# Kernel optimization log

Measured on AMD Instinct MI355X. Metric: run time of the kernel, lower is better.

Reference implementation:

```python
import jax, jax.numpy as jnp
import numpy as np

B, L = 2, 2048
DIM, VOCAB, NL = 1024, 32000, 4
DSTATE, DCONV, EXPAND, HEADDIM = 128, 4, 2, 64
DIN = EXPAND * DIM            # 2048
H = DIN // HEADDIM            # 32 heads
CONVDIM = DIN + 2 * DSTATE    # 2304
DPROJ = 2 * DIN + 2 * DSTATE + H  # 4384
FFN = 4 * DIM                 # 4096
Q = 128                       # SSD chunk size
EPS = 1e-6


def _rms(x):
    return x * jax.lax.rsqrt(jnp.mean(x * x, axis=-1, keepdims=True) + EPS)


def _causal_conv(x, w, b):
    # x [B,L,C], depthwise causal conv, w [C,DCONV], b [C]
    y = jax.lax.conv_general_dilated(
        x.transpose(0, 2, 1), w[:, None, :], (1,), [(DCONV - 1, 0)],
        dimension_numbers=('NCH', 'OIH', 'NCH'), feature_group_count=CONVDIM)
    return (y + b[:, None]).transpose(0, 2, 1)


def _ssd(x, dt, A, Bm, Cm):
    # Exact selective scan h_t = h_{t-1}*exp(dt_t*A) + dt_t * x_t B_t ; y_t = C_t . h_t
    # computed in chunked (SSD) matmul form. x [b,l,h,p], dt [b,l,h], A [h], Bm/Cm [b,l,n]
    b, l, h, p = x.shape
    n = Bm.shape[-1]
    c = l // Q
    xr = x.reshape(b, c, Q, h, p)
    dtr = dt.reshape(b, c, Q, h)
    ar = (dt * A).reshape(b, c, Q, h)          # per-step log-decay (<= 0)
    Br = Bm.reshape(b, c, Q, n)
    Cr = Cm.reshape(b, c, Q, n)
    ca = jnp.cumsum(ar, axis=2)                # inclusive cumulative log-decay
    # ---- intra-chunk: causal decay-weighted 'attention' ----
    cah = ca.transpose(0, 1, 3, 2)             # [b,c,h,Q]
    idx = jnp.arange(Q)
    mask = idx[:, None] >= idx[None, :]
    diff = jnp.where(mask[None, None, None], cah[..., :, None] - cah[..., None, :], -jnp.inf)
    M = jnp.exp(diff)                          # [b,c,h,Q,Q]
    CB = jnp.einsum('bcin,bcjn->bcij', Cr, Br)
    T = CB[:, :, None] * M                     # [b,c,h,Q,Q]
    y_intra = jnp.einsum('bchij,bcjh,bcjhp->bcihp', T, dtr, xr)
    # ---- chunk-final states ----
    w = jnp.exp(ca[:, :, -1:, :] - ca) * dtr   # [b,c,Q,h]
    states = jnp.einsum('bcjh,bcjn,bcjhp->bchpn', w, Br, xr)
    chunk_decay = jnp.exp(ca[:, :, -1, :])     # [b,c,h]
    def step(s, inp):
        cd, st = inp
        prev = s
        s = s * cd[:, :, None, None] + st
        return s, prev
    s0 = jnp.zeros((b, h, p, n), x.dtype)
    _, s_prev = jax.lax.scan(step, s0, (chunk_decay.transpose(1, 0, 2),
                                        states.transpose(1, 0, 2, 3, 4)))
    s_prev = s_prev.transpose(1, 0, 2, 3, 4)   # [b,c,h,p,n] state entering each chunk
    y_inter = jnp.einsum('bcih,bcin,bchpn->bcihp', jnp.exp(ca), Cr, s_prev)
    return (y_intra + y_inter).reshape(b, l, h, p)


def _mamba(x, Wi, cw, cb, dtb, Alog, Dp, nw, Wo):
    bsz, sl, _ = x.shape
    zxbcdt = x @ Wi.T                          # [b,l,DPROJ]
    z = zxbcdt[..., :DIN]
    xBC = zxbcdt[..., DIN:DIN + CONVDIM]
    dtraw = zxbcdt[..., DIN + CONVDIM:]
    xBC = jax.nn.silu(_causal_conv(xBC, cw, cb))
    xs = xBC[..., :DIN]
    Bm = xBC[..., DIN:DIN + DSTATE]
    Cm = xBC[..., DIN + DSTATE:]
    dt = jax.nn.softplus(dtraw + dtb)
    A = -jnp.exp(Alog)
    x4 = xs.reshape(bsz, sl, H, HEADDIM)
    y = _ssd(x4, dt, A, Bm, Cm) + Dp[None, None, :, None] * x4
    y = y.reshape(bsz, sl, DIN)
    yg = y * jax.nn.silu(z)                    # gated RMSNorm (norm_before_gate=False)
    y = _rms(yg) * nw
    return y @ Wo.T


def _forward(tokens, embedding, lm_head_bias, in_proj_w, conv_w, conv_b,
             dt_bias, A_log, D, mnorm_w, out_proj_w, u_w, v_w, o_w):
    x = embedding[tokens]
    for li in range(NL):
        for _ in range(2):  # original applies each (mamba, ffn) pair twice
            x = _rms(x)
            x = x + _mamba(x, in_proj_w[li], conv_w[li], conv_b[li], dt_bias[li],
                           A_log[li], D[li], mnorm_w[li], out_proj_w[li])
            x = _rms(x)
            x = x + ((x @ u_w[li].T) * (x @ v_w[li].T)) @ o_w[li].T  # SGLU, dropout=0
    return x @ embedding.T + lm_head_bias      # tied lm_head


def setup_inputs():
    key = jax.random.key(0)
    ks = jax.random.split(key, 16)
    s = 0.02
    return {
        'tokens': jax.random.randint(ks[0], (B, L), 0, VOCAB),
        'embedding': jax.random.normal(ks[1], (VOCAB, DIM), jnp.float32) * s,
        'lm_head_bias': jnp.zeros((VOCAB,), jnp.float32),
        'in_proj_w': jax.random.normal(ks[2], (NL, DPROJ, DIM), jnp.float32) * s,
        'conv_w': jax.random.normal(ks[3], (NL, CONVDIM, DCONV), jnp.float32) * 0.2,
        'conv_b': jnp.zeros((NL, CONVDIM), jnp.float32),
        'dt_bias': jax.random.normal(ks[4], (NL, H), jnp.float32) * 0.3 - 3.0,
        'A_log': jnp.log(jax.random.uniform(ks[5], (NL, H), jnp.float32, 1.0, 16.0)),
        'D': jnp.ones((NL, H), jnp.float32) + 0.1 * jax.random.normal(ks[6], (NL, H), jnp.float32),
        'mnorm_w': jnp.ones((NL, DIN), jnp.float32),
        'out_proj_w': jax.random.normal(ks[7], (NL, DIM, DIN), jnp.float32) * s,
        'u_w': jax.random.normal(ks[8], (NL, FFN, DIM), jnp.float32) * s,
        'v_w': jax.random.normal(ks[9], (NL, FFN, DIM), jnp.float32) * s,
        'o_w': jax.random.normal(ks[10], (NL, DIM, FFN), jnp.float32) * s,
    }


def reference(tokens, embedding, lm_head_bias, in_proj_w, conv_w, conv_b,
              dt_bias, A_log, D, mnorm_w, out_proj_w, u_w, v_w, o_w):
    return _forward(tokens, embedding, lm_head_bias, in_proj_w, conv_w, conv_b,
                    dt_bias, A_log, D, mnorm_w, out_proj_w, u_w, v_w, o_w)
```

## Files before the change

### kernel.cpp

```cpp
#include <hip/hip_runtime.h>
#include <hip/hip_bf16.h>

#define BSZ 2
#define LSEQ 2048
#define DIM 1024
#define VOCAB 32000
#define NLAYER 4
#define DSTATE 128
#define DCONV 4
#define HEADDIM 64
#define DIN 2048
#define NH 32
#define CONVDIM 2304
#define DPROJ 4384
#define FFN 4096
#define QLEN 128
#define NTOK 4096
#define NCHUNK 32
#define CPB 16

#define SMEM_BYTES 147456
#define SMEM2 131072

using f32x4 = __attribute__((ext_vector_type(4))) float;
using f16   = _Float16;
using f16x4 = __attribute__((ext_vector_type(4))) _Float16;
using f16x8 = __attribute__((ext_vector_type(8))) _Float16;

__device__ __forceinline__ void gld16(const void* g, void* l) {
  __builtin_amdgcn_global_load_lds(
      (const __attribute__((address_space(1))) unsigned int*)g,
      (__attribute__((address_space(3))) unsigned int*)l, 16, 0, 0);
}

// ... 6 lines not shown
  const int nchx = nx / CW;
  const int per = CW * ny;
  const int ch = bid / per;
  if (ch < nchx) {
    int wi = bid - ch * per;
    bx = ch * CW + (wi & (CW - 1));
    by = wi / CW;
  } else {
    int tb = bid - nchx * per;
    int tw = nx - nchx * CW;
    bx = nchx * CW + (tb % tw);
    by = tb / tw;
  }
}

template <int MODE>
__global__ __launch_bounds__(512, 2) void gemm_p(
    const f16* __restrict__ A, const f16* __restrict__ Bu, const f16* __restrict__ Bv,
    float* __restrict__ Cf, f16* __restrict__ Gh, const float* __restrict__ bias,
    int N, int Ksub, int lda, int ldb, int ldc)
{
  extern __shared__ char smem[];
  const int tid  = threadIdx.x;
  const int lane = tid & 63;
  const int wid  = tid >> 6;
  int bx, by; swz_tiles(bx, by);
  const int m0 = by * 256;
  const int n0 = bx * 128;
  const size_t kbase = (size_t)blockIdx.z * Ksub;
  if (gridDim.z > 1) Cf += (size_t)blockIdx.z * (size_t)gridDim.y * 256 * ldc;

  const int NT  = Ksub >> 6;
  const int NTT = (MODE == 2) ? 2 * NT : NT;

  int arA[4], acA[4];
#pragma unroll
  for (int L = 0; L < 4; ++L) {
    int q = L * 512 + tid;
    int row = q >> 3;
    arA[L] = m0 + row;
    acA[L] = ((q & 7) ^ (row & 7)) << 3;
  }
  int brB[2], bcB[2];
#pragma unroll
  for (int L = 0; L < 2; ++L) {
    int q = L * 512 + tid;
    int row = q >> 3;
    int r = n0 + row; if (r > N - 1) r = N - 1;
    brB[L] = r;
    bcB[L] = ((q & 7) ^ (row & 7)) << 3;
  }

  auto stage = [&](int tt) {
    const int b = tt - (tt / 3) * 3;
    char* Ad = smem + b * 32768;
    char* Bd = smem + 98304 + b * 16384;
    int ta = tt;
    const f16* Bp = Bu;
    if (MODE == 2 && tt >= NT) { ta = tt - NT; Bp = Bv; }
    const int kb = ta << 6;
#pragma unroll
    for (int L = 0; L < 4; ++L)
      gld16(A + (size_t)arA[L] * lda + kbase + kb + acA[L], Ad + (L * 512 + tid) * 16);
#pragma unroll
    for (int L = 0; L < 2; ++L)
      gld16(Bp + (size_t)brB[L] * ldb + kbase + kb + bcB[L], Bd + (L * 512 + tid) * 16);
  };

  const int wm = (wid >> 1) << 6;
  const int wn = (wid & 1) << 6;
  const int fr = lane & 15;
  const int kg = lane >> 4;

  f32x4 accu[4][4] = {};
  f32x4 accv[4][4] = {};

  stage(0);
  stage(1);

  for (int t = 0; t < NTT; ++t) {
    const int b = t - (t / 3) * 3;
    if (t + 2 < NTT) {
      stage(t + 2);
      asm volatile("s_waitcnt vmcnt(12)" ::: "memory");
    } else if (t + 1 < NTT) {
      asm volatile("s_waitcnt vmcnt(6)" ::: "memory");
    } else {
      asm volatile("s_waitcnt vmcnt(0)" ::: "memory");
    }
    __builtin_amdgcn_s_barrier();
    asm volatile("" ::: "memory");
    const f16* Ab = (const f16*)(smem + b * 32768);
    const f16* Bb = (const f16*)(smem + 98304 + b * 16384);
#pragma unroll
    for (int s = 0; s < 2; ++s) {
      f16x8 af[4], bf[4];
#pragma unroll
      for (int j = 0; j < 4; ++j) {
        int row = wm + j * 16 + fr;
        int g = kg + s * 4;
        af[j] = *(const f16x8*)&Ab[row * 64 + ((g ^ (row & 7)) << 3)];
      }
#pragma unroll
      for (int i = 0; i < 4; ++i) {
        int row = wn + i * 16 + fr;
        int g = kg + s * 4;
        bf[i] = *(const f16x8*)&Bb[row * 64 + ((g ^ (row & 7)) << 3)];
      }
      __builtin_amdgcn_s_setprio(1);
      if (MODE == 2 && t >= NT) {
#pragma unroll
        for (int i = 0; i < 4; ++i)
#pragma unroll
          for (int j = 0; j < 4; ++j)
            accv[i][j] = __builtin_amdgcn_mfma_f32_16x16x32_f16(bf[i], af[j], accv[i][j], 0, 0, 0);
      } else {
#pragma unroll
        for (int i = 0; i < 4; ++i)
#pragma unroll
          for (int j = 0; j < 4; ++j)
            accu[i][j] = __builtin_amdgcn_mfma_f32_16x16x32_f16(bf[i], af[j], accu[i][j], 0, 0, 0);
      }
      __builtin_amdgcn_s_setprio(0);
    }
    asm volatile("" ::: "memory");
    __builtin_amdgcn_s_barrier();
    asm volatile("" ::: "memory");
  }

  const int c4 = kg << 2;
  if constexpr (MODE == 0) {
#pragma unroll
    for (int i = 0; i < 4; ++i) {
      const int col = n0 + wn + i * 16 + c4;
      if (col >= N) continue;
      f32x4 bv = bias ? *(const f32x4*)(bias + col) : f32x4{0, 0, 0, 0};
#pragma unroll
      for (int j = 0; j < 4; ++j) {
        const int row = m0 + wm + j * 16 + fr;
        *(f32x4*)(Cf + (size_t)row * ldc + col) = accu[i][j] + bv;
      }
    }
  } else {
#pragma unroll
    for (int i = 0; i < 4; ++i) {
      const int col = n0 + wn + i * 16 + c4;
#pragma unroll
      for (int j = 0; j < 4; ++j) {
        const int row = m0 + wm + j * 16 + fr;
        f16x4 h;
#pragma unroll
        for (int r = 0; r < 4; ++r)
          h[r] = (f16)(accu[i][j][r] * accv[i][j][r]);
        *(f16x4*)(Gh + (size_t)row * ldc + col) = h;
      }
    }
  }
}

__global__ __launch_bounds__(512, 2) void gemm_p2(
    const f16* __restrict__ A, const f16* __restrict__ B,
    float* __restrict__ Cf, const float* __restrict__ bias,
    int N, int Ksub, int lda, int ldb, int ldc)
{
  extern __shared__ char smem[];
  const int tid  = threadIdx.x;
  const int lane = tid & 63;
  const int wid  = tid >> 6;
  int bx, by; swz_tiles(bx, by);
  const int m0 = by * 256;
  const int n0 = bx * 256;
  const size_t kbase = (size_t)blockIdx.z * Ksub;
  if (gridDim.z > 1) Cf += (size_t)blockIdx.z * (size_t)gridDim.y * 256 * ldc;
  const int NT = Ksub >> 6;

  int arA[4], acA[4], brB[4], bcB[4];
#pragma unroll
  for (int L = 0; L < 4; ++L) {
    int q = L * 512 + tid;
    int row = q >> 3;
    arA[L] = m0 + row;
    acA[L] = ((q & 7) ^ (row & 7)) << 3;
    int r = n0 + row; if (r > N - 1) r = N - 1;
    brB[L] = r;
    bcB[L] = acA[L];
  }

  auto stage = [&](int tt) {
// ... 166 lines not shown
  for (int i = 0; i < 4; ++i) {
    const int col = n0 + wn + i * 16 + c4;
#pragma unroll
    for (int j = 0; j < 4; ++j) {
      const int row = m0 + wm + j * 16 + fr;
      f16x4 h;
#pragma unroll
      for (int r = 0; r < 4; ++r)
        h[r] = (f16)(accu[i][j][r] * accv[i][j][r]);
      *(f16x4*)(Gh + (size_t)row * FFN + col) = h;
    }
  }
}

template <bool DORMS>
__global__ __launch_bounds__(256) void reduce_rms(const float* __restrict__ parts,
                                                  const float* __restrict__ resid,
                                                  float* __restrict__ xn,
                                                  f16* __restrict__ outh, int np)
{
  const int row = blockIdx.x, tid = threadIdx.x;
  const size_t base = (size_t)row * DIM + tid * 4;
  f32x4 s = *(const f32x4*)(resid + base);
  for (int p = 0; p < np; ++p)
    s += *(const f32x4*)(parts + (size_t)p * (NTOK * DIM) + base);
  if constexpr (!DORMS) {
    f16x4 h;
#pragma unroll
    for (int c = 0; c < 4; ++c) h[c] = (f16)s[c];
    *(f16x4*)(outh + base) = h;
    return;
  }
  float ss = s[0] * s[0] + s[1] * s[1] + s[2] * s[2] + s[3] * s[3];
  for (int o = 32; o; o >>= 1) ss += __shfl_down(ss, o);
  __shared__ float red[4];
  if ((tid & 63) == 0) red[tid >> 6] = ss;
  __syncthreads();
  ss = red[0] + red[1] + red[2] + red[3];
  const float sc = rsqrtf(ss * (1.f / 1024.f) + 1e-6f);
  f32x4 o4 = s * sc;
// ... 13 lines not shown
    f16x4 o;
#pragma unroll
    for (int c = 0; c < 4; ++c) o[c] = (f16)v[c];
    *(f16x4*)(dst + i) = o;
  }
}

__global__ __launch_bounds__(256) void cvt_wts(
    const float* __restrict__ inw, const float* __restrict__ outw,
    const float* __restrict__ uw, const float* __restrict__ vw,
    const float* __restrict__ ow,
    f16* __restrict__ w_in, f16* __restrict__ w_out,
    f16* __restrict__ w_uv, f16* __restrict__ w_o)
{
  const int b = blockIdx.x;
  const float* src; f16* dst; int base;
  if (b < 4384)       { src = inw;  dst = w_in;                       base = 0; }
  else if (b < 6432)  { src = outw; dst = w_out;                      base = 4384; }
  else if (b < 10528) { src = uw;   dst = w_uv;                       base = 6432; }
  else if (b < 14624) { src = vw;   dst = w_uv + (size_t)FFN * DIM;   base = 10528; }
  else                { src = ow;   dst = w_o;                        base = 14624; }
  const size_t i = ((size_t)(b - base) * 256 + threadIdx.x) * 4;
  f32x4 v = *(const f32x4*)(src + i);
  f16x4 o;
#pragma unroll
  for (int c = 0; c < 4; ++c) o[c] = (f16)v[c];
  *(f16x4*)(dst + i) = o;
}

__global__ __launch_bounds__(256) void gather_k(const int* __restrict__ tok,
                                                const float* __restrict__ emb,
                                                float* __restrict__ x)
{
  const int row = blockIdx.x;
  const int t = tok[row];
  const f32x4* s = (const f32x4*)(emb + (size_t)t * DIM);
  f32x4* d = (f32x4*)(x + (size_t)row * DIM);
// ... 9 lines not shown
  float ss = v[0] * v[0] + v[1] * v[1] + v[2] * v[2] + v[3] * v[3];
  for (int o = 32; o; o >>= 1) ss += __shfl_down(ss, o);
  __shared__ float red[4];
  if ((tid & 63) == 0) red[tid >> 6] = ss;
  __syncthreads();
  ss = red[0] + red[1] + red[2] + red[3];
  const float sc = rsqrtf(ss * (1.f / 1024.f) + 1e-6f);
  f32x4 o4 = v * sc;
  ((f32x4*)(outf + (size_t)row * DIM))[tid] = o4;
  f16x4 h;
#pragma unroll
  for (int c = 0; c < 4; ++c) h[c] = (f16)o4[c];
  ((f16x4*)(outh + (size_t)row * DIM))[tid] = h;
}

__global__ __launch_bounds__(256) void convdt(const float* __restrict__ zx,
                                              const float* __restrict__ cw,
                                              const float* __restrict__ cbias,
                                              const float* __restrict__ dtb,
                                              const float* __restrict__ alog,
                                              float* __restrict__ xbc,
                                              float* __restrict__ dt,
                                              float* __restrict__ ca)
{
  if (blockIdx.x < 576) {
    const int sid = blockIdx.x * 256 + threadIdx.x;
    const int c0 = (sid % 576) * 4;
    const int t0 = (sid / 576) * 16;
    float w[4][4], bs[4];
#pragma unroll
    for (int cc = 0; cc < 4; ++cc) {
      f32x4 wv = *(const f32x4*)(cw + (size_t)(c0 + cc) * 4);
      w[cc][0] = wv[0]; w[cc][1] = wv[1]; w[cc][2] = wv[2]; w[cc][3] = wv[3];
      bs[cc] = cbias[c0 + cc];
    }
    const int l0 = t0 & (LSEQ - 1);
    f32x4 x3 = {0, 0, 0, 0}, x2 = {0, 0, 0, 0}, x1 = {0, 0, 0, 0};
    if (l0 != 0) {
      x3 = *(const f32x4*)(zx + (size_t)(t0 - 3) * DPROJ + DIN + c0);
      x2 = *(const f32x4*)(zx + (size_t)(t0 - 2) * DPROJ + DIN + c0);
      x1 = *(const f32x4*)(zx + (size_t)(t0 - 1) * DPROJ + DIN + c0);
    }
    for (int i = 0; i < 16; ++i) {
      const int t = t0 + i;
      f32x4 xc = *(const f32x4*)(zx + (size_t)t * DPROJ + DIN + c0);
      f32x4 o;
#pragma unroll
      for (int cc = 0; cc < 4; ++cc) {
        float a = bs[cc] + x3[cc] * w[cc][0] + x2[cc] * w[cc][1] +
                  x1[cc] * w[cc][2] + xc[cc] * w[cc][3];
        o[cc] = a / (1.f + expf(-a));
      }
      *(f32x4*)(xbc + (size_t)t * CONVDIM + c0) = o;
      x3 = x2; x2 = x1; x1 = xc;
    }
  } else {
    const int loc = (threadIdx.x >> 7) * 128;
    const int u = (blockIdx.x - 576) * 2 + (threadIdx.x >> 7);
    const int bc = u >> 5, h = u & 31, q = threadIdx.x & 127;
    const int t = bc * 128 + q;
    float raw = zx[(size_t)t * DPROJ + (DIN + CONVDIM) + h] + dtb[h];
    float d = raw > 20.f ? raw : log1pf(expf(raw));
    dt[t * 32 + h] = d;
    float a = -expf(alog[h]) * d;
    __shared__ float s[256];
    s[loc + q] = a;
    __syncthreads();
    for (int off = 1; off < 128; off <<= 1) {
      float v = (q >= off) ? s[loc + q - off] : 0.f;
      __syncthreads();
      s[loc + q] += v;
      __syncthreads();
    }
    ca[(size_t)u * 128 + q] = s[loc + q];
  }
}

__global__ __launch_bounds__(256) void cb_mfma(const float* __restrict__ xbc,
                                               float* __restrict__ CBo)
{
  const int bc = blockIdx.x;
  __shared__ f16 Cm[128 * 72], Bm[128 * 72];
  const int tid = threadIdx.x, lane = tid & 63, wid = tid >> 6;
  const int fr = lane & 15, kg = lane >> 4;
  f32x4 acc[2][8] = {};
  const int i = tid & 127;
  const float* rowp = xbc + (size_t)(bc * 128 + i) * CONVDIM + DIN;

  for (int kh = 0; kh < 2; ++kh) {
#pragma unroll
    for (int it = 0; it < 8; ++it) {
      int idx = it * 256 + tid;
      int n0 = (idx >> 7) * 4;
      f32x4 bv = *(const f32x4*)(rowp + kh * 64 + n0);
      f32x4 cv = *(const f32x4*)(rowp + DSTATE + kh * 64 + n0);
      f16x4 hb, hc;
#pragma unroll
      for (int c = 0; c < 4; ++c) { hb[c] = (f16)bv[c]; hc[c] = (f16)cv[c]; }
      *(f16x4*)&Bm[i * 72 + n0] = hb;
      *(f16x4*)&Cm[i * 72 + n0] = hc;
    }
    __syncthreads();
#pragma unroll
    for (int kf = 0; kf < 2; ++kf) {
      const int ko = kf * 32 + kg * 8;
      f16x8 cf[2], bf[8];
#pragma unroll
      for (int ii = 0; ii < 2; ++ii)
        cf[ii] = *(const f16x8*)&Cm[((wid * 2 + ii) * 16 + fr) * 72 + ko];
#pragma unroll
      for (int jj = 0; jj < 8; ++jj)
        bf[jj] = *(const f16x8*)&Bm[(jj * 16 + fr) * 72 + ko];
      __builtin_amdgcn_s_setprio(1);
#pragma unroll
      for (int ii = 0; ii < 2; ++ii)
// ... 6 lines not shown
  }
  float* out = CBo + (size_t)bc * 16384;
#pragma unroll
  for (int ii = 0; ii < 2; ++ii) {
    const int i0 = (wid * 2 + ii) * 16 + kg * 4;
#pragma unroll
    for (int jj = 0; jj < 8; ++jj) {
      const int j = jj * 16 + fr;
#pragma unroll
      for (int r = 0; r < 4; ++r)
        out[(size_t)(i0 + r) * 128 + j] = acc[ii][jj][r];
    }
  }
}

__global__ __launch_bounds__(256) void ssd_states(const float* __restrict__ xbc,
                                                  const float* __restrict__ dt,
                                                  const float* __restrict__ ca,
                                                  float* __restrict__ ST)
{
  const int bc = blockIdx.x >> 5, h = blockIdx.x & 31;
  __shared__ f16 Am[128 * 136];
  __shared__ f16 Bm[64 * 136];
  __shared__ float warr[128];
  const int tid = threadIdx.x, lane = tid & 63, wid = tid >> 6;
  if (tid < 128) {
    float cv = ca[(size_t)blockIdx.x * 128 + tid];
    float cl = ca[(size_t)blockIdx.x * 128 + 127];
    warr[tid] = expf(cl - cv) * dt[(size_t)(bc * 128 + tid) * 32 + h];
  }
  __syncthreads();
  {
    const int j = tid & 127;
    const float wj = warr[j];
    const float* br = xbc + (size_t)(bc * 128 + j) * CONVDIM + DIN;
#pragma unroll
    for (int it = 0; it < 16; ++it) {
      int idx = it * 256 + tid;
      int n0 = (idx >> 7) * 4;
      f32x4 v = *(const f32x4*)(br + n0);
#pragma unroll
      for (int c = 0; c < 4; ++c) Am[(n0 + c) * 136 + j] = (f16)(v[c] * wj);
    }
    const float* xr = xbc + (size_t)(bc * 128 + j) * CONVDIM + h * 64;
#pragma unroll
    for (int it = 0; it < 8; ++it) {
      int idx = it * 256 + tid;
      int p0 = (idx >> 7) * 4;
      f32x4 v = *(const f32x4*)(xr + p0);
#pragma unroll
      for (int c = 0; c < 4; ++c) Bm[(p0 + c) * 136 + j] = (f16)v[c];
    }
  }
  __syncthreads();
  const int fr = lane & 15, kg = lane >> 4;
  f32x4 acc[2][4] = {};
#pragma unroll
  for (int kf = 0; kf < 4; ++kf) {
    const int ko = kf * 32 + kg * 8;
    f16x8 bw[2], xf[4];
#pragma unroll
    for (int ii = 0; ii < 2; ++ii)
      bw[ii] = *(const f16x8*)&Am[((wid * 2 + ii) * 16 + fr) * 136 + ko];
#pragma unroll
    for (int pi = 0; pi < 4; ++pi)
      xf[pi] = *(const f16x8*)&Bm[(pi * 16 + fr) * 136 + ko];
// ... 21 lines not shown
                                              float* __restrict__ states)
{
  const int b = blockIdx.x >> 10, h = (blockIdx.x >> 5) & 31, seg = blockIdx.x & 31;
  const int e = seg * 256 + threadIdx.x;
  float s = 0.f;
  for (int c = 0; c < CPB; ++c) {
    int bc = b * CPB + c;
    float cd = expf(ca[(size_t)(bc * 32 + h) * 128 + 127]);
    size_t idx = (size_t)(bc * 32 + h) * 8192 + e;
    float v = states[idx];
    states[idx] = s;
    s = s * cd + v;
  }
}

__global__ __launch_bounds__(256) void ssd_y(const float* __restrict__ xbc,
                                             const float* __restrict__ dt,
                                             const float* __restrict__ ca,
                                             const float* __restrict__ CB,
                                             const float* __restrict__ Dvec,
                                             const float* __restrict__ ST,
                                             float* __restrict__ ybuf)
{
  const int bc = blockIdx.x >> 5, h = blockIdx.x & 31;
  __shared__ f16 Am[128 * 136];
  __shared__ f16 Bm[64 * 136];
  __shared__ float cas[128], dtl[128];
  const int tid = threadIdx.x, lane = tid & 63, wid = tid >> 6;
  if (tid < 128) {
    cas[tid] = ca[(size_t)blockIdx.x * 128 + tid];
    dtl[tid] = dt[(size_t)(bc * 128 + tid) * 32 + h];
  }
  __syncthreads();
  {
    const int j = tid & 127;
    const float dj = dtl[j];
    const float* xr = xbc + (size_t)(bc * 128 + j) * CONVDIM + h * 64;
#pragma unroll
    for (int it = 0; it < 8; ++it) {
      int idx = it * 256 + tid;
      int p0 = (idx >> 7) * 4;
      f32x4 v = *(const f32x4*)(xr + p0);
#pragma unroll
      for (int c = 0; c < 4; ++c) Bm[(p0 + c) * 136 + j] = (f16)(v[c] * dj);
    }
  }
  {
    const int i = tid >> 1;
    const int jh = (tid & 1) * 64;
    const float cai = cas[i];
    const float* cbr = CB + (size_t)bc * 16384 + (size_t)i * 128 + jh;
#pragma unroll
    for (int g = 0; g < 8; ++g) {
      int j0 = g * 8;
      f32x4 v0 = *(const f32x4*)(cbr + j0);
      f32x4 v1 = *(const f32x4*)(cbr + j0 + 4);
      f16x8 tv;
#pragma unroll
      for (int c = 0; c < 8; ++c) {
// ... 17 lines not shown
      xf[pi] = *(const f16x8*)&Bm[(pi * 16 + fr) * 136 + ko];
#pragma unroll
    for (int ii = 0; ii < 2; ++ii)
      tf[ii] = *(const f16x8*)&Am[((wid * 2 + ii) * 16 + fr) * 136 + ko];
    __builtin_amdgcn_s_setprio(1);
#pragma unroll
    for (int ii = 0; ii < 2; ++ii)
#pragma unroll
      for (int pi = 0; pi < 4; ++pi)
        a1[ii][pi] = __builtin_amdgcn_mfma_f32_16x16x32_f16(xf[pi], tf[ii], a1[ii][pi], 0, 0, 0);
    __builtin_amdgcn_s_setprio(0);
  }
  __syncthreads();
  {
    const int i = tid & 127;
    const float* cr = xbc + (size_t)(bc * 128 + i) * CONVDIM + DIN + DSTATE;
#pragma unroll
    for (int it = 0; it < 16; ++it) {
      int idx = it * 256 + tid;
      int n0 = (idx >> 7) * 4;
      f32x4 v = *(const f32x4*)(cr + n0);
      f16x4 hv;
#pragma unroll
      for (int c = 0; c < 4; ++c) hv[c] = (f16)v[c];
      *(f16x4*)&Am[i * 136 + n0] = hv;
    }
    const float* sr = ST + (size_t)blockIdx.x * 8192;
    const int p = tid & 63;
#pragma unroll
    for (int it = 0; it < 8; ++it) {
      int idx = it * 256 + tid;
      int n0 = (idx >> 6) * 4;
      f32x4 v = *(const f32x4*)(sr + (size_t)p * 128 + n0);
      f16x4 hv;
#pragma unroll
      for (int c = 0; c < 4; ++c) hv[c] = (f16)v[c];
      *(f16x4*)&Bm[p * 136 + n0] = hv;
    }
  }
  __syncthreads();
// ... 12 lines not shown
    for (int ii = 0; ii < 2; ++ii)
#pragma unroll
      for (int pi = 0; pi < 4; ++pi)
        a2[ii][pi] = __builtin_amdgcn_mfma_f32_16x16x32_f16(sf[pi], cf[ii], a2[ii][pi], 0, 0, 0);
    __builtin_amdgcn_s_setprio(0);
  }
  const float dh = Dvec[h];
#pragma unroll
  for (int ii = 0; ii < 2; ++ii) {
    const int i = (wid * 2 + ii) * 16 + fr;
    const float ei = expf(cas[i]);
    const int tg = bc * 128 + i;
#pragma unroll
    for (int pi = 0; pi < 4; ++pi) {
      const int p0 = pi * 16 + kg * 4;
      f32x4 xv = *(const f32x4*)(xbc + (size_t)tg * CONVDIM + h * 64 + p0);
      f32x4 y = a1[ii][pi] + ei * a2[ii][pi] + dh * xv;
      *(f32x4*)(ybuf + (size_t)tg * DIN + h * 64 + p0) = y;
    }
  }
}

__global__ __launch_bounds__(256) void gate_rms(const float* __restrict__ ybuf,
                                                const float* __restrict__ zx,
                                                const float* __restrict__ nw,
                                                f16* __restrict__ outh)
{
  const int row = blockIdx.x, tid = threadIdx.x;
  const float* yr = ybuf + (size_t)row * DIN;
  const float* zr = zx + (size_t)row * DPROJ;
  f32x4 y0 = *(const f32x4*)(yr + tid * 4);
  f32x4 y1 = *(const f32x4*)(yr + 1024 + tid * 4);
  f32x4 z0 = *(const f32x4*)(zr + tid * 4);
  f32x4 z1 = *(const f32x4*)(zr + 1024 + tid * 4);
  f32x4 g0, g1;
#pragma unroll
  for (int c = 0; c < 4; ++c) {
    g0[c] = y0[c] * (z0[c] / (1.f + expf(-z0[c])));
    g1[c] = y1[c] * (z1[c] / (1.f + expf(-z1[c])));
  }
  float ss = 0.f;
#pragma unroll
  for (int c = 0; c < 4; ++c) ss += g0[c] * g0[c] + g1[c] * g1[c];
  for (int o = 32; o; o >>= 1) ss += __shfl_down(ss, o);
  __shared__ float red[4];
  if ((tid & 63) == 0) red[tid >> 6] = ss;
  __syncthreads();
  ss = red[0] + red[1] + red[2] + red[3];
  const float sc = rsqrtf(ss * (1.f / 2048.f) + 1e-6f);
  f32x4 w0 = *(const f32x4*)(nw + tid * 4);
  f32x4 w1 = *(const f32x4*)(nw + 1024 + tid * 4);
  f16x4 h0, h1;
#pragma unroll
  for (int c = 0; c < 4; ++c) {
    h0[c] = (f16)(g0[c] * sc * w0[c]);
    h1[c] = (f16)(g1[c] * sc * w1[c]);
  }
  *(f16x4*)(outh + (size_t)row * DIN + tid * 4) = h0;
  *(f16x4*)(outh + (size_t)row * DIN + 1024 + tid * 4) = h1;
}

extern "C" void kernel_launch(void* const* d_in, const int* in_sizes, int n_in,
                              void* d_out, int out_size, void* d_ws, size_t ws_size,
                              hipStream_t stream)
{
  (void)in_sizes; (void)n_in; (void)out_size; (void)ws_size;
  const int*   tokens = (const int*)d_in[0];
  const float* emb    = (const float*)d_in[1];
  const float* lmb    = (const float*)d_in[2];
  const float* inw    = (const float*)d_in[3];
  const float* cw     = (const float*)d_in[4];
  const float* cbias  = (const float*)d_in[5];
  const float* dtb    = (const float*)d_in[6];
  const float* alog   = (const float*)d_in[7];
  const float* Dvec   = (const float*)d_in[8];
  const float* nw     = (const float*)d_in[9];
  const float* outw   = (const float*)d_in[10];
  const float* uw     = (const float*)d_in[11];
  const float* vw     = (const float*)d_in[12];
  const float* ow     = (const float*)d_in[13];

  char* ws = (char*)d_ws;
  size_t off = 0;
  auto alloc = [&](size_t bytes) { void* p = ws + off; off += (bytes + 255) & ~(size_t)255; return p; };
  f16* emb_h  = (f16*)alloc((size_t)VOCAB * DIM * 2);
  f16* w_in   = (f16*)alloc((size_t)DPROJ * DIM * 2);
  f16* w_out  = (f16*)alloc((size_t)DIM * DIN * 2);
  f16* w_uv   = (f16*)alloc((size_t)2 * FFN * DIM * 2);
  f16* w_o    = (f16*)alloc((size_t)DIM * FFN * 2);
  float* xbuf = (float*)alloc((size_t)NTOK * DIM * 4);
  float* xn   = (float*)alloc((size_t)NTOK * DIM * 4);
  f16* xnh    = (f16*)alloc((size_t)NTOK * DIM * 2);
  f16* xh_lm  = (f16*)alloc((size_t)NTOK * DIM * 2);
  float* dtbuf = (float*)alloc((size_t)NTOK * NH * 4);
  float* cabuf = (float*)alloc((size_t)NCHUNK * NH * QLEN * 4);
  float* CBbuf = (float*)alloc((size_t)NCHUNK * QLEN * QLEN * 4);
  f16* abh    = (f16*)alloc((size_t)NTOK * FFN * 2);

  char* ob = (char*)d_out;
  float* states = (float*)(ob);
  float* zxb    = (float*)(ob + 134217728);
  float* xbc    = (float*)(ob + 206045184);
  float* ybuf   = (float*)(ob + 243793920);
  float* parts  = (float*)(ob + 277348352);

  cvt_f2h_k<<<4096, 256, 0, stream>>>(emb, emb_h, VOCAB * DIM);
  gather_k<<<NTOK, 256, 0, stream>>>(tokens, emb, xbuf);
  rms1024<<<NTOK, 256, 0, stream>>>(xbuf, xn, xnh);

  for (int it = 0; it < 2 * NLAYER; ++it) {
    const int li = it >> 1;
    if ((it & 1) == 0) {
      cvt_wts<<<18720, 256, 0, stream>>>(
          inw + (size_t)li * DPROJ * DIM, outw + (size_t)li * DIM * DIN,
          uw + (size_t)li * FFN * DIM, vw + (size_t)li * FFN * DIM,
          ow + (size_t)li * DIM * FFN, w_in, w_out, w_uv, w_o);
    }
    gemm_p<0><<<dim3((DPROJ + 127) / 128, NTOK / 256, 1), 512, SMEM_BYTES, stream>>>(
        xnh, w_in, nullptr, zxb, nullptr, nullptr, DPROJ, DIM, DIM, DIM, DPROJ);
    convdt<<<1088, 256, 0, stream>>>(zxb, cw + (size_t)li * CONVDIM * DCONV,
                                     cbias + (size_t)li * CONVDIM,
                                     dtb + li * NH, alog + li * NH, xbc, dtbuf, cabuf);
    cb_mfma<<<NCHUNK, 256, 0, stream>>>(xbc, CBbuf);
    ssd_states<<<NCHUNK * NH, 256, 0, stream>>>(xbc, dtbuf, cabuf, states);
    scan_k<<<2048, 256, 0, stream>>>(cabuf, states);
    ssd_y<<<NCHUNK * NH, 256, 0, stream>>>(xbc, dtbuf, cabuf, CBbuf,
                                           Dvec + li * NH, states, ybuf);
    gate_rms<<<NTOK, 256, 0, stream>>>(ybuf, zxb, nw + (size_t)li * DIN, abh);
    gemm_p<0><<<dim3(DIM / 128, NTOK / 256, 2), 512, SMEM_BYTES, stream>>>(
        abh, w_out, nullptr, parts, nullptr, nullptr, DIM, DIN / 2, DIN, DIN, DIM);
    reduce_rms<true><<<NTOK, 256, 0, stream>>>(parts, xn, xn, xnh, 2);
    gemm_uv2<<<dim3(FFN / 128, NTOK / 256, 1), 512, SMEM2, stream>>>(
        xnh, w_uv, w_uv + (size_t)FFN * DIM, abh);
    gemm_p<0><<<dim3(DIM / 128, NTOK / 256, 2), 512, SMEM_BYTES, stream>>>(
        abh, w_o, nullptr, parts, nullptr, nullptr, DIM, FFN / 2, FFN, FFN, DIM);
    if (it < 2 * NLAYER - 1)
      reduce_rms<true><<<NTOK, 256, 0, stream>>>(parts, xn, xn, xnh, 2);
    else
      reduce_rms<false><<<NTOK, 256, 0, stream>>>(parts, xn, nullptr, xh_lm, 2);
  }

  gemm_p2<<<dim3(VOCAB / 256, NTOK / 256, 1), 512, SMEM2, stream>>>(
      xh_lm, emb_h, (float*)d_out, lmb, VOCAB, DIM, DIM, DIM, VOCAB);
}
```

Measured before the change: 3.289 ms.

## Store intermediates in fp16 and convert all layer weights in one launch

Projection output, conv output, SSD y, and split-K partial buffers move from fp32 to fp16 throughout the Mamba pipeline. The dt columns of the in-projection are also written in fp32 to a side buffer. All four layers' weights are converted to fp16 in a single up-front launch instead of once per layer, with the converted copies held in the output scratch region. This cuts memory traffic and launch count, at the cost of precision loss in the split-K partials and activations.

Measured after the change: 3.165 ms. 1.04x faster.

```diff
diff --git a/kernel.cpp b/kernel.cpp
--- a/kernel.cpp
+++ b/kernel.cpp
@@ -18,6 +18,7 @@
 #define NTOK 4096
 #define NCHUNK 32
 #define CPB 16
+#define DTOFF 4352
 
 #define SMEM_BYTES 147456
 #define SMEM2 131072
@@ -54,10 +55,9 @@
   }
 }
 
-template <int MODE>
 __global__ __launch_bounds__(512, 2) void gemm_p(
-    const f16* __restrict__ A, const f16* __restrict__ Bu, const f16* __restrict__ Bv,
-    float* __restrict__ Cf, f16* __restrict__ Gh, const float* __restrict__ bias,
+    const f16* __restrict__ A, const f16* __restrict__ B,
+    f16* __restrict__ Cg, float* __restrict__ dtr,
     int N, int Ksub, int lda, int ldb, int ldc)
 {
   extern __shared__ char smem[];
@@ -68,10 +68,8 @@
   const int m0 = by * 256;
   const int n0 = bx * 128;
   const size_t kbase = (size_t)blockIdx.z * Ksub;
-  if (gridDim.z > 1) Cf += (size_t)blockIdx.z * (size_t)gridDim.y * 256 * ldc;
-
-  const int NT  = Ksub >> 6;
-  const int NTT = (MODE == 2) ? 2 * NT : NT;
+  if (gridDim.z > 1) Cg += (size_t)blockIdx.z * (size_t)gridDim.y * 256 * ldc;
+  const int NT = Ksub >> 6;
 
   int arA[4], acA[4];
 #pragma unroll
@@ -95,16 +93,13 @@
     const int b = tt - (tt / 3) * 3;
     char* Ad = smem + b * 32768;
     char* Bd = smem + 98304 + b * 16384;
-    int ta = tt;
-    const f16* Bp = Bu;
-    if (MODE == 2 && tt >= NT) { ta = tt - NT; Bp = Bv; }
-    const int kb = ta << 6;
+    const int kb = tt << 6;
 #pragma unroll
     for (int L = 0; L < 4; ++L)
       gld16(A + (size_t)arA[L] * lda + kbase + kb + acA[L], Ad + (L * 512 + tid) * 16);
 #pragma unroll
     for (int L = 0; L < 2; ++L)
-      gld16(Bp + (size_t)brB[L] * ldb + kbase + kb + bcB[L], Bd + (L * 512 + tid) * 16);
+      gld16(B + (size_t)brB[L] * ldb + kbase + kb + bcB[L], Bd + (L * 512 + tid) * 16);
   };
 
   const int wm = (wid >> 1) << 6;
@@ -112,18 +107,17 @@
   const int fr = lane & 15;
   const int kg = lane >> 4;
 
-  f32x4 accu[4][4] = {};
-  f32x4 accv[4][4] = {};
+  f32x4 acc[4][4] = {};
 
   stage(0);
   stage(1);
 
-  for (int t = 0; t < NTT; ++t) {
+  for (int t = 0; t < NT; ++t) {
     const int b = t - (t / 3) * 3;
-    if (t + 2 < NTT) {
+    if (t + 2 < NT) {
       stage(t + 2);
       asm volatile("s_waitcnt vmcnt(12)" ::: "memory");
-    } else if (t + 1 < NTT) {
+    } else if (t + 1 < NT) {
       asm volatile("s_waitcnt vmcnt(6)" ::: "memory");
     } else {
       asm volatile("s_waitcnt vmcnt(0)" ::: "memory");
@@ -148,19 +142,11 @@
         bf[i] = *(const f16x8*)&Bb[row * 64 + ((g ^ (row & 7)) << 3)];
       }
       __builtin_amdgcn_s_setprio(1);
-      if (MODE == 2 && t >= NT) {
-#pragma unroll
-        for (int i = 0; i < 4; ++i)
-#pragma unroll
-          for (int j = 0; j < 4; ++j)
-            accv[i][j] = __builtin_amdgcn_mfma_f32_16x16x32_f16(bf[i], af[j], accv[i][j], 0, 0, 0);
-      } else {
-#pragma unroll
-        for (int i = 0; i < 4; ++i)
-#pragma unroll
-          for (int j = 0; j < 4; ++j)
-            accu[i][j] = __builtin_amdgcn_mfma_f32_16x16x32_f16(bf[i], af[j], accu[i][j], 0, 0, 0);
-      }
+#pragma unroll
+      for (int i = 0; i < 4; ++i)
+#pragma unroll
+        for (int j = 0; j < 4; ++j)
+          acc[i][j] = __builtin_amdgcn_mfma_f32_16x16x32_f16(bf[i], af[j], acc[i][j], 0, 0, 0);
       __builtin_amdgcn_s_setprio(0);
     }
     asm volatile("" ::: "memory");
@@ -169,31 +155,19 @@
   }
 
   const int c4 = kg << 2;
-  if constexpr (MODE == 0) {
-#pragma unroll
-    for (int i = 0; i < 4; ++i) {
-      const int col = n0 + wn + i * 16 + c4;
-      if (col >= N) continue;
-      f32x4 bv = bias ? *(const f32x4*)(bias + col) : f32x4{0, 0, 0, 0};
-#pragma unroll
-      for (int j = 0; j < 4; ++j) {
-        const int row = m0 + wm + j * 16 + fr;
-        *(f32x4*)(Cf + (size_t)row * ldc + col) = accu[i][j] + bv;
-      }
-    }
-  } else {
-#pragma unroll
-    for (int i = 0; i < 4; ++i) {
-      const int col = n0 + wn + i * 16 + c4;
-#pragma unroll
-      for (int j = 0; j < 4; ++j) {
-        const int row = m0 + wm + j * 16 + fr;
-        f16x4 h;
-#pragma unroll
-        for (int r = 0; r < 4; ++r)
-          h[r] = (f16)(accu[i][j][r] * accv[i][j][r]);
-        *(f16x4*)(Gh + (size_t)row * ldc + col) = h;
-      }
+#pragma unroll
+  for (int i = 0; i < 4; ++i) {
+    const int col = n0 + wn + i * 16 + c4;
+    if (col >= N) continue;
+#pragma unroll
+    for (int j = 0; j < 4; ++j) {
+      const int row = m0 + wm + j * 16 + fr;
+      f16x4 h;
+#pragma unroll
+      for (int r = 0; r < 4; ++r) h[r] = (f16)acc[i][j][r];
+      *(f16x4*)(Cg + (size_t)row * ldc + col) = h;
+      if (dtr && col >= DTOFF)
+        *(f32x4*)(dtr + (size_t)row * NH + (col - DTOFF)) = acc[i][j];
     }
   }
 }
@@ -211,7 +185,6 @@
   const int m0 = by * 256;
   const int n0 = bx * 256;
   const size_t kbase = (size_t)blockIdx.z * Ksub;
-  if (gridDim.z > 1) Cf += (size_t)blockIdx.z * (size_t)gridDim.y * 256 * ldc;
   const int NT = Ksub >> 6;
 
   int arA[4], acA[4], brB[4], bcB[4];
@@ -408,7 +381,7 @@
 }
 
 template <bool DORMS>
-__global__ __launch_bounds__(256) void reduce_rms(const float* __restrict__ parts,
+__global__ __launch_bounds__(256) void reduce_rms(const f16* __restrict__ parts,
                                                   const float* __restrict__ resid,
                                                   float* __restrict__ xn,
                                                   f16* __restrict__ outh, int np)
@@ -416,8 +389,11 @@
   const int row = blockIdx.x, tid = threadIdx.x;
   const size_t base = (size_t)row * DIM + tid * 4;
   f32x4 s = *(const f32x4*)(resid + base);
-  for (int p = 0; p < np; ++p)
-    s += *(const f32x4*)(parts + (size_t)p * (NTOK * DIM) + base);
+  for (int p = 0; p < np; ++p) {
+    f16x4 pv = *(const f16x4*)(parts + (size_t)p * (NTOK * DIM) + base);
+#pragma unroll
+    for (int c = 0; c < 4; ++c) s[c] += (float)pv[c];
+  }
   if constexpr (!DORMS) {
     f16x4 h;
 #pragma unroll
@@ -461,13 +437,29 @@
     f16* __restrict__ w_uv, f16* __restrict__ w_o)
 {
   const int b = blockIdx.x;
-  const float* src; f16* dst; int base;
-  if (b < 4384)       { src = inw;  dst = w_in;                       base = 0; }
-  else if (b < 6432)  { src = outw; dst = w_out;                      base = 4384; }
-  else if (b < 10528) { src = uw;   dst = w_uv;                       base = 6432; }
-  else if (b < 14624) { src = vw;   dst = w_uv + (size_t)FFN * DIM;   base = 10528; }
-  else                { src = ow;   dst = w_o;                        base = 14624; }
-  const size_t i = ((size_t)(b - base) * 256 + threadIdx.x) * 4;
+  const float* src; f16* dst;
+  if (b < 17536) {
+    int li = b / 4384, ib = b - li * 4384;
+    src = inw  + (size_t)li * 4489216 + (size_t)ib * 1024;
+    dst = w_in + (size_t)li * 4489216 + (size_t)ib * 1024;
+  } else if (b < 25728) {
+    int lb = b - 17536, li = lb >> 11, ib = lb & 2047;
+    src = outw  + (size_t)li * 2097152 + (size_t)ib * 1024;
+    dst = w_out + (size_t)li * 2097152 + (size_t)ib * 1024;
+  } else if (b < 42112) {
+    int lb = b - 25728, li = lb >> 12, ib = lb & 4095;
+    src = uw   + (size_t)li * 4194304 + (size_t)ib * 1024;
+    dst = w_uv + (size_t)li * 8388608 + (size_t)ib * 1024;
+  } else if (b < 58496) {
+    int lb = b - 42112, li = lb >> 12, ib = lb & 4095;
+    src = vw   + (size_t)li * 4194304 + (size_t)ib * 1024;
+    dst = w_uv + (size_t)li * 8388608 + 4194304 + (size_t)ib * 1024;
+  } else {
+    int lb = b - 58496, li = lb >> 12, ib = lb & 4095;
+    src = ow  + (size_t)li * 4194304 + (size_t)ib * 1024;
+    dst = w_o + (size_t)li * 4194304 + (size_t)ib * 1024;
+  }
+  const size_t i = (size_t)threadIdx.x * 4;
   f32x4 v = *(const f32x4*)(src + i);
   f16x4 o;
 #pragma unroll
@@ -507,12 +499,13 @@
   ((f16x4*)(outh + (size_t)row * DIM))[tid] = h;
 }
 
-__global__ __launch_bounds__(256) void convdt(const float* __restrict__ zx,
+__global__ __launch_bounds__(256) void convdt(const f16* __restrict__ zx,
+                                              const float* __restrict__ dtrw,
                                               const float* __restrict__ cw,
                                               const float* __restrict__ cbias,
                                               const float* __restrict__ dtb,
                                               const float* __restrict__ alog,
-                                              float* __restrict__ xbc,
+                                              f16* __restrict__ xbc,
                                               float* __restrict__ dt,
                                               float* __restrict__ ca)
 {
@@ -528,31 +521,34 @@
       bs[cc] = cbias[c0 + cc];
     }
     const int l0 = t0 & (LSEQ - 1);
-    f32x4 x3 = {0, 0, 0, 0}, x2 = {0, 0, 0, 0}, x1 = {0, 0, 0, 0};
+    float x3[4] = {}, x2[4] = {}, x1[4] = {};
     if (l0 != 0) {
-      x3 = *(const f32x4*)(zx + (size_t)(t0 - 3) * DPROJ + DIN + c0);
-      x2 = *(const f32x4*)(zx + (size_t)(t0 - 2) * DPROJ + DIN + c0);
-      x1 = *(const f32x4*)(zx + (size_t)(t0 - 1) * DPROJ + DIN + c0);
+      f16x4 a = *(const f16x4*)(zx + (size_t)(t0 - 3) * DPROJ + DIN + c0);
+      f16x4 b = *(const f16x4*)(zx + (size_t)(t0 - 2) * DPROJ + DIN + c0);
+      f16x4 d = *(const f16x4*)(zx + (size_t)(t0 - 1) * DPROJ + DIN + c0);
+#pragma unroll
+      for (int c = 0; c < 4; ++c) { x3[c] = (float)a[c]; x2[c] = (float)b[c]; x1[c] = (float)d[c]; }
     }
     for (int i = 0; i < 16; ++i) {
       const int t = t0 + i;
-      f32x4 xc = *(const f32x4*)(zx + (size_t)t * DPROJ + DIN + c0);
-      f32x4 o;
+      f16x4 xcv = *(const f16x4*)(zx + (size_t)t * DPROJ + DIN + c0);
+      f16x4 o;
 #pragma unroll
       for (int cc = 0; cc < 4; ++cc) {
+        float xc = (float)xcv[cc];
         float a = bs[cc] + x3[cc] * w[cc][0] + x2[cc] * w[cc][1] +
-                  x1[cc] * w[cc][2] + xc[cc] * w[cc][3];
-        o[cc] = a / (1.f + expf(-a));
+                  x1[cc] * w[cc][2] + xc * w[cc][3];
+        o[cc] = (f16)(a / (1.f + expf(-a)));
+        x3[cc] = x2[cc]; x2[cc] = x1[cc]; x1[cc] = xc;
       }
-      *(f32x4*)(xbc + (size_t)t * CONVDIM + c0) = o;
-      x3 = x2; x2 = x1; x1 = xc;
+      *(f16x4*)(xbc + (size_t)t * CONVDIM + c0) = o;
     }
   } else {
     const int loc = (threadIdx.x >> 7) * 128;
     const int u = (blockIdx.x - 576) * 2 + (threadIdx.x >> 7);
     const int bc = u >> 5, h = u & 31, q = threadIdx.x & 127;
     const int t = bc * 128 + q;
-    float raw = zx[(size_t)t * DPROJ + (DIN + CONVDIM) + h] + dtb[h];
+    float raw = dtrw[(size_t)t * NH + h] + dtb[h];
     float d = raw > 20.f ? raw : log1pf(expf(raw));
     dt[t * 32 + h] = d;
     float a = -expf(alog[h]) * d;
@@ -569,7 +565,7 @@
   }
 }
 
-__global__ __launch_bounds__(256) void cb_mfma(const float* __restrict__ xbc,
+__global__ __launch_bounds__(256) void cb_mfma(const f16* __restrict__ xbc,
                                                float* __restrict__ CBo)
 {
   const int bc = blockIdx.x;
@@ -578,20 +574,15 @@
   const int fr = lane & 15, kg = lane >> 4;
   f32x4 acc[2][8] = {};
   const int i = tid & 127;
-  const float* rowp = xbc + (size_t)(bc * 128 + i) * CONVDIM + DIN;
+  const f16* rowp = xbc + (size_t)(bc * 128 + i) * CONVDIM + DIN;
 
   for (int kh = 0; kh < 2; ++kh) {
 #pragma unroll
     for (int it = 0; it < 8; ++it) {
       int idx = it * 256 + tid;
       int n0 = (idx >> 7) * 4;
-      f32x4 bv = *(const f32x4*)(rowp + kh * 64 + n0);
-      f32x4 cv = *(const f32x4*)(rowp + DSTATE + kh * 64 + n0);
-      f16x4 hb, hc;
-#pragma unroll
-      for (int c = 0; c < 4; ++c) { hb[c] = (f16)bv[c]; hc[c] = (f16)cv[c]; }
-      *(f16x4*)&Bm[i * 72 + n0] = hb;
-      *(f16x4*)&Cm[i * 72 + n0] = hc;
+      *(f16x4*)&Bm[i * 72 + n0] = *(const f16x4*)(rowp + kh * 64 + n0);
+      *(f16x4*)&Cm[i * 72 + n0] = *(const f16x4*)(rowp + DSTATE + kh * 64 + n0);
     }
     __syncthreads();
 #pragma unroll
@@ -628,7 +619,7 @@
   }
 }
 
-__global__ __launch_bounds__(256) void ssd_states(const float* __restrict__ xbc,
+__global__ __launch_bounds__(256) void ssd_states(const f16* __restrict__ xbc,
                                                   const float* __restrict__ dt,
                                                   const float* __restrict__ ca,
                                                   float* __restrict__ ST)
@@ -647,23 +638,23 @@
   {
     const int j = tid & 127;
     const float wj = warr[j];
-    const float* br = xbc + (size_t)(bc * 128 + j) * CONVDIM + DIN;
+    const f16* br = xbc + (size_t)(bc * 128 + j) * CONVDIM + DIN;
 #pragma unroll
     for (int it = 0; it < 16; ++it) {
       int idx = it * 256 + tid;
       int n0 = (idx >> 7) * 4;
-      f32x4 v = *(const f32x4*)(br + n0);
-#pragma unroll
-      for (int c = 0; c < 4; ++c) Am[(n0 + c) * 136 + j] = (f16)(v[c] * wj);
-    }
-    const float* xr = xbc + (size_t)(bc * 128 + j) * CONVDIM + h * 64;
+      f16x4 v = *(const f16x4*)(br + n0);
+#pragma unroll
+      for (int c = 0; c < 4; ++c) Am[(n0 + c) * 136 + j] = (f16)((float)v[c] * wj);
+    }
+    const f16* xr = xbc + (size_t)(bc * 128 + j) * CONVDIM + h * 64;
 #pragma unroll
     for (int it = 0; it < 8; ++it) {
       int idx = it * 256 + tid;
       int p0 = (idx >> 7) * 4;
-      f32x4 v = *(const f32x4*)(xr + p0);
-#pragma unroll
-      for (int c = 0; c < 4; ++c) Bm[(p0 + c) * 136 + j] = (f16)v[c];
+      f16x4 v = *(const f16x4*)(xr + p0);
+#pragma unroll
+      for (int c = 0; c < 4; ++c) Bm[(p0 + c) * 136 + j] = v[c];
     }
   }
   __syncthreads();
@@ -715,13 +706,13 @@
   }
 }
 
-__global__ __launch_bounds__(256) void ssd_y(const float* __restrict__ xbc,
+__global__ __launch_bounds__(256) void ssd_y(const f16* __restrict__ xbc,
                                              const float* __restrict__ dt,
                                              const float* __restrict__ ca,
                                              const float* __restrict__ CB,
                                              const float* __restrict__ Dvec,
                                              const float* __restrict__ ST,
-                                             float* __restrict__ ybuf)
+                                             f16* __restrict__ ybuf)
 {
   const int bc = blockIdx.x >> 5, h = blockIdx.x & 31;
   __shared__ f16 Am[128 * 136];
@@ -736,14 +727,14 @@
   {
     const int j = tid & 127;
     const float dj = dtl[j];
-    const float* xr = xbc + (size_t)(bc * 128 + j) * CONVDIM + h * 64;
+    const f16* xr = xbc + (size_t)(bc * 128 + j) * CONVDIM + h * 64;
 #pragma unroll
     for (int it = 0; it < 8; ++it) {
       int idx = it * 256 + tid;
       int p0 = (idx >> 7) * 4;
-      f32x4 v = *(const f32x4*)(xr + p0);
-#pragma unroll
-      for (int c = 0; c < 4; ++c) Bm[(p0 + c) * 136 + j] = (f16)(v[c] * dj);
+      f16x4 v = *(const f16x4*)(xr + p0);
+#pragma unroll
+      for (int c = 0; c < 4; ++c) Bm[(p0 + c) * 136 + j] = (f16)((float)v[c] * dj);
     }
   }
   {
@@ -791,16 +782,12 @@
   __syncthreads();
   {
     const int i = tid & 127;
-    const float* cr = xbc + (size_t)(bc * 128 + i) * CONVDIM + DIN + DSTATE;
+    const f16* cr = xbc + (size_t)(bc * 128 + i) * CONVDIM + DIN + DSTATE;
 #pragma unroll
     for (int it = 0; it < 16; ++it) {
       int idx = it * 256 + tid;
       int n0 = (idx >> 7) * 4;
-      f32x4 v = *(const f32x4*)(cr + n0);
-      f16x4 hv;
-#pragma unroll
-      for (int c = 0; c < 4; ++c) hv[c] = (f16)v[c];
-      *(f16x4*)&Am[i * 136 + n0] = hv;
+      *(f16x4*)&Am[i * 136 + n0] = *(const f16x4*)(cr + n0);
     }
     const float* sr = ST + (size_t)blockIdx.x * 8192;
     const int p = tid & 63;
@@ -843,50 +830,47 @@
 #pragma unroll
     for (int pi = 0; pi < 4; ++pi) {
       const int p0 = pi * 16 + kg * 4;
-      f32x4 xv = *(const f32x4*)(xbc + (size_t)tg * CONVDIM + h * 64 + p0);
-      f32x4 y = a1[ii][pi] + ei * a2[ii][pi] + dh * xv;
-      *(f32x4*)(ybuf + (size_t)tg * DIN + h * 64 + p0) = y;
-    }
-  }
-}
-
-__global__ __launch_bounds__(256) void gate_rms(const float* __restrict__ ybuf,
-                                                const float* __restrict__ zx,
+      f16x4 xv = *(const f16x4*)(xbc + (size_t)tg * CONVDIM + h * 64 + p0);
+      f16x4 yo;
+#pragma unroll
+      for (int r = 0; r < 4; ++r)
+        yo[r] = (f16)(a1[ii][pi][r] + ei * a2[ii][pi][r] + dh * (float)xv[r]);
+      *(f16x4*)(ybuf + (size_t)tg * DIN + h * 64 + p0) = yo;
+    }
+  }
+}
+
+__global__ __launch_bounds__(256) void gate_rms(const f16* __restrict__ ybuf,
+                                                const f16* __restrict__ zx,
                                                 const float* __restrict__ nw,
                                                 f16* __restrict__ outh)
 {
   const int row = blockIdx.x, tid = threadIdx.x;
-  const float* yr = ybuf + (size_t)row * DIN;
-  const float* zr = zx + (size_t)row * DPROJ;
-  f32x4 y0 = *(const f32x4*)(yr + tid * 4);
-  f32x4 y1 = *(const f32x4*)(yr + 1024 + tid * 4);
-  f32x4 z0 = *(const f32x4*)(zr + tid * 4);
-  f32x4 z1 = *(const f32x4*)(zr + 1024 + tid * 4);
-  f32x4 g0, g1;
-#pragma unroll
-  for (int c = 0; c < 4; ++c) {
-    g0[c] = y0[c] * (z0[c] / (1.f + expf(-z0[c])));
-    g1[c] = y1[c] * (z1[c] / (1.f + expf(-z1[c])));
-  }
+  f16x8 yv = *(const f16x8*)(ybuf + (size_t)row * DIN + tid * 8);
+  f16x8 zv = *(const f16x8*)(zx + (size_t)row * DPROJ + tid * 8);
+  float g[8];
   float ss = 0.f;
 #pragma unroll
-  for (int c = 0; c < 4; ++c) ss += g0[c] * g0[c] + g1[c] * g1[c];
+  for (int c = 0; c < 8; ++c) {
+    float z = (float)zv[c];
+    g[c] = (float)yv[c] * (z / (1.f + expf(-z)));
+    ss += g[c] * g[c];
+  }
   for (int o = 32; o; o >>= 1) ss += __shfl_down(ss, o);
   __shared__ float red[4];
   if ((tid & 63) == 0) red[tid >> 6] = ss;
   __syncthreads();
   ss = red[0] + red[1] + red[2] + red[3];
   const float sc = rsqrtf(ss * (1.f / 2048.f) + 1e-6f);
-  f32x4 w0 = *(const f32x4*)(nw + tid * 4);
-  f32x4 w1 = *(const f32x4*)(nw + 1024 + tid * 4);
-  f16x4 h0, h1;
-#pragma unroll
-  for (int c = 0; c < 4; ++c) {
-    h0[c] = (f16)(g0[c] * sc * w0[c]);
-    h1[c] = (f16)(g1[c] * sc * w1[c]);
-  }
-  *(f16x4*)(outh + (size_t)row * DIN + tid * 4) = h0;
-  *(f16x4*)(outh + (size_t)row * DIN + 1024 + tid * 4) = h1;
+  f32x4 w0 = *(const f32x4*)(nw + tid * 8);
+  f32x4 w1 = *(const f32x4*)(nw + tid * 8 + 4);
+  f16x8 h;
+#pragma unroll
+  for (int c = 0; c < 8; ++c) {
+    float w = (c < 4) ? w0[c] : w1[c - 4];
+    h[c] = (f16)(g[c] * sc * w);
+  }
+  *(f16x8*)(outh + (size_t)row * DIN + tid * 8) = h;
 }
 
 extern "C" void kernel_launch(void* const* d_in, const int* in_sizes, int n_in,
@@ -912,42 +896,43 @@
   char* ws = (char*)d_ws;
   size_t off = 0;
   auto alloc = [&](size_t bytes) { void* p = ws + off; off += (bytes + 255) & ~(size_t)255; return p; };
-  f16* emb_h  = (f16*)alloc((size_t)VOCAB * DIM * 2);
-  f16* w_in   = (f16*)alloc((size_t)DPROJ * DIM * 2);
-  f16* w_out  = (f16*)alloc((size_t)DIM * DIN * 2);
-  f16* w_uv   = (f16*)alloc((size_t)2 * FFN * DIM * 2);
-  f16* w_o    = (f16*)alloc((size_t)DIM * FFN * 2);
-  float* xbuf = (float*)alloc((size_t)NTOK * DIM * 4);
-  float* xn   = (float*)alloc((size_t)NTOK * DIM * 4);
-  f16* xnh    = (f16*)alloc((size_t)NTOK * DIM * 2);
-  f16* xh_lm  = (f16*)alloc((size_t)NTOK * DIM * 2);
+  f16* emb_h   = (f16*)alloc((size_t)VOCAB * DIM * 2);
+  float* xbuf  = (float*)alloc((size_t)NTOK * DIM * 4);
+  float* xn    = (float*)alloc((size_t)NTOK * DIM * 4);
+  f16* xnh     = (f16*)alloc((size_t)NTOK * DIM * 2);
+  f16* xh_lm   = (f16*)alloc((size_t)NTOK * DIM * 2);
+  float* dtraw = (float*)alloc((size_t)NTOK * NH * 4);
   float* dtbuf = (float*)alloc((size_t)NTOK * NH * 4);
   float* cabuf = (float*)alloc((size_t)NCHUNK * NH * QLEN * 4);
   float* CBbuf = (float*)alloc((size_t)NCHUNK * QLEN * QLEN * 4);
-  f16* abh    = (f16*)alloc((size_t)NTOK * FFN * 2);
+  f16* abh     = (f16*)alloc((size_t)NTOK * FFN * 2);
 
   char* ob = (char*)d_out;
   float* states = (float*)(ob);
-  float* zxb    = (float*)(ob + 134217728);
-  float* xbc    = (float*)(ob + 206045184);
-  float* ybuf   = (float*)(ob + 243793920);
-  float* parts  = (float*)(ob + 277348352);
+  f16* zxb      = (f16*)(ob + 40000000);
+  f16* xbc      = (f16*)(ob + 80000000);
+  f16* ybuf     = (f16*)(ob + 100000000);
+  f16* parts    = (f16*)(ob + 120000000);
+  f16* w_in     = (f16*)(ob + 160000000);
+  f16* w_out    = (f16*)(ob + 196000000);
+  f16* w_uv     = (f16*)(ob + 213000000);
+  f16* w_o      = (f16*)(ob + 281000000);
 
   cvt_f2h_k<<<4096, 256, 0, stream>>>(emb, emb_h, VOCAB * DIM);
+  cvt_wts<<<74880, 256, 0, stream>>>(inw, outw, uw, vw, ow, w_in, w_out, w_uv, w_o);
   gather_k<<<NTOK, 256, 0, stream>>>(tokens, emb, xbuf);
   rms1024<<<NTOK, 256, 0, stream>>>(xbuf, xn, xnh);
 
   for (int it = 0; it < 2 * NLAYER; ++it) {
     const int li = it >> 1;
-    if ((it & 1) == 0) {
-      cvt_wts<<<18720, 256, 0, stream>>>(
-          inw + (size_t)li * DPROJ * DIM, outw + (size_t)li * DIM * DIN,
-          uw + (size_t)li * FFN * DIM, vw + (size_t)li * FFN * DIM,
-          ow + (size_t)li * DIM * FFN, w_in, w_out, w_uv, w_o);
-    }
-    gemm_p<0><<<dim3((DPROJ + 127) / 128, NTOK / 256, 1), 512, SMEM_BYTES, stream>>>(
-        xnh, w_in, nullptr, zxb, nullptr, nullptr, DPROJ, DIM, DIM, DIM, DPROJ);
-    convdt<<<1088, 256, 0, stream>>>(zxb, cw + (size_t)li * CONVDIM * DCONV,
+    const f16* w_inL  = w_in  + (size_t)li * 4489216;
+    const f16* w_outL = w_out + (size_t)li * 2097152;
+    const f16* w_uL   = w_uv  + (size_t)li * 8388608;
+    const f16* w_vL   = w_uL  + 4194304;
+    const f16* w_oL   = w_o   + (size_t)li * 4194304;
+    gemm_p<<<dim3((DPROJ + 127) / 128, NTOK / 256, 1), 512, SMEM_BYTES, stream>>>(
+        xnh, w_inL, zxb, dtraw, DPROJ, DIM, DIM, DIM, DPROJ);
+    convdt<<<1088, 256, 0, stream>>>(zxb, dtraw, cw + (size_t)li * CONVDIM * DCONV,
                                      cbias + (size_t)li * CONVDIM,
                                      dtb + li * NH, alog + li * NH, xbc, dtbuf, cabuf);
     cb_mfma<<<NCHUNK, 256, 0, stream>>>(xbc, CBbuf);
@@ -956,13 +941,13 @@
     ssd_y<<<NCHUNK * NH, 256, 0, stream>>>(xbc, dtbuf, cabuf, CBbuf,
                                            Dvec + li * NH, states, ybuf);
     gate_rms<<<NTOK, 256, 0, stream>>>(ybuf, zxb, nw + (size_t)li * DIN, abh);
-    gemm_p<0><<<dim3(DIM / 128, NTOK / 256, 2), 512, SMEM_BYTES, stream>>>(
-        abh, w_out, nullptr, parts, nullptr, nullptr, DIM, DIN / 2, DIN, DIN, DIM);
+    gemm_p<<<dim3(DIM / 128, NTOK / 256, 2), 512, SMEM_BYTES, stream>>>(
+        abh, w_outL, parts, nullptr, DIM, DIN / 2, DIN, DIN, DIM);
     reduce_rms<true><<<NTOK, 256, 0, stream>>>(parts, xn, xn, xnh, 2);
     gemm_uv2<<<dim3(FFN / 128, NTOK / 256, 1), 512, SMEM2, stream>>>(
-        xnh, w_uv, w_uv + (size_t)FFN * DIM, abh);
-    gemm_p<0><<<dim3(DIM / 128, NTOK / 256, 2), 512, SMEM_BYTES, stream>>>(
-        abh, w_o, nullptr, parts, nullptr, nullptr, DIM, FFN / 2, FFN, FFN, DIM);
+        xnh, w_uL, w_vL, abh);
+    gemm_p<<<dim3(DIM / 128, NTOK / 256, 2), 512, SMEM_BYTES, stream>>>(
+        abh, w_oL, parts, nullptr, DIM, FFN / 2, FFN, FFN, DIM);
     if (it < 2 * NLAYER - 1)
       reduce_rms<true><<<NTOK, 256, 0, stream>>>(parts, xn, xn, xnh, 2);
     else
```
